# Optimization experiments

Hardware: AMD Instinct MI355X
Metric: run time of the kernel (lower is better)

The kernel has to match this reference:

```python
import jax, jax.numpy as jnp
import numpy as np

BLOCK = 32  # GGUF Q8_0 block size: one scale per 32 int8 quants


def setup_inputs() -> dict:
    key = jax.random.key(0)
    k1, k2, k3, k4 = jax.random.split(key, 4)
    B, S, D_IN, D_OUT = 2, 2048, 4096, 16384
    x = jax.random.normal(k1, (B, S, D_IN), dtype=jnp.float32)
    # Stored quantized weights: unsigned byte codes in [0,255]; dequant as (q-128)*scale
    weight_q = jax.random.randint(k2, (D_OUT, D_IN), 0, 255, dtype=jnp.int32)
    # One positive scale per 32-element block along in_features
    scales = jax.random.uniform(k3, (D_OUT, D_IN // BLOCK), dtype=jnp.float32) * 0.02 + 1e-3
    bias = jax.random.normal(k4, (D_OUT,), dtype=jnp.float32)
    return {"x": x, "weight_q": weight_q, "scales": scales, "bias": bias}


def _dequant(weight_q, scales):
    # weight_q: [O, I] int codes, scales: [O, I/BLOCK] -> fp weight [O, I]
    O, I = weight_q.shape
    q = (weight_q.astype(jnp.float32) - 128.0).reshape(O, I // BLOCK, BLOCK)
    return (q * scales[:, :, None]).reshape(O, I)


def reference(x, weight_q, scales, bias):
    # Fused dequant + matmul: y = x @ dequant(W).T + bias
    w = _dequant(weight_q, scales)  # [O, I]
    y = jnp.einsum("bsi,oi->bso", x, w)
    return y + bias
```

## Files before the change

### kernel.cpp

```cpp
#include <hip/hip_runtime.h>
#include <hip/hip_bf16.h>

typedef __attribute__((ext_vector_type(8))) short short8;
typedef __attribute__((ext_vector_type(4))) float f32x4;
typedef __attribute__((ext_vector_type(16))) float f32x16;

#define AS1 __attribute__((address_space(1)))
#define AS3 __attribute__((address_space(3)))

static __device__ __forceinline__ short f2bf(float f) {
    __hip_bfloat16 h = __float2bfloat16(f);
    union { __hip_bfloat16 h; short s; } u;
    u.h = h;
    return u.s;
}


__global__ __launch_bounds__(256) void prepack_w_kernel(const int* __restrict__ wq,
                                                        const float* __restrict__ scales,
                                                        short* __restrict__ Wb,
                                                        long total8) {
    long i = (long)blockIdx.x * 256 + threadIdx.x;
    if (i >= total8) return;
    const int4* p = (const int4*)wq + i * 2;
    int4 q0 = p[0], q1 = p[1];
    float s = scales[(i * 8) >> 5];
    short8 v;
    v[0] = f2bf((float)(q0.x - 128) * s);
    v[1] = f2bf((float)(q0.y - 128) * s);
    v[2] = f2bf((float)(q0.z - 128) * s);
    v[3] = f2bf((float)(q0.w - 128) * s);
    v[4] = f2bf((float)(q1.x - 128) * s);
    v[5] = f2bf((float)(q1.y - 128) * s);
    v[6] = f2bf((float)(q1.z - 128) * s);
    v[7] = f2bf((float)(q1.w - 128) * s);
    ((short8*)Wb)[i] = v;
}

__global__ __launch_bounds__(256) void prepack_x_kernel(const float* __restrict__ x,
                                                        short* __restrict__ Xb,
                                                        long total8) {
    long i = (long)blockIdx.x * 256 + threadIdx.x;
    if (i >= total8) return;
    const float4* p = (const float4*)x + i * 2;
    float4 f0 = p[0], f1 = p[1];
    short8 v;
    v[0] = f2bf(f0.x); v[1] = f2bf(f0.y); v[2] = f2bf(f0.z); v[3] = f2bf(f0.w);
    v[4] = f2bf(f1.x); v[5] = f2bf(f1.y); v[6] = f2bf(f1.z); v[7] = f2bf(f1.w);
    ((short8*)Xb)[i] = v;
}

__global__ __launch_bounds__(512, 2)
void gemm256_kernel(const float* __restrict__ bias,
                    const short* __restrict__ Xb, const short* __restrict__ Wb,
                    float* __restrict__ out, int M, int N, int K) {
    __shared__ alignas(16) short As[4 * 8192];
    __shared__ alignas(16) short Bs[4 * 8192];

    const int nM = M >> 8, nN = N >> 8;
    int bid = blockIdx.x;
    {
        int nwg = nM * nN;
        if ((nwg & 7) == 0) bid = (bid & 7) * (nwg >> 3) + (bid >> 3);
    }
    int pm, pn;
    {
        const int G = 8;
        if ((nN % G) == 0) {
            int per = nM * G;
            int grp = bid / per, in = bid % per;
            pn = grp * G + (in % G);
            pm = in / G;
        } else { pn = bid % nN; pm = bid / nN; }
    }

    const int tid  = threadIdx.x;
    const int lane = tid & 63;
    const int wid  = tid >> 6;
    const int wm   = wid >> 2;
    const int wn   = wid & 3;
    const int l31  = lane & 31;
    const int l5   = lane >> 5;
    const int lx   = lane & 7;

    const long bm = (long)pm << 8, bn = (long)pn << 8;
    const long Kl = K;
    const int  NT = K >> 6;

    const int aslot0 = wm * 8192,        aslot1 = (2 + wm) * 8192;
    const int bslot0 = (wn >> 1) * 8192 + ((wn & 1) * 64) * 64;
    const int bslot1 = bslot0 + 2 * 8192;
    const int frow   = l31 * 64;
    const int sgk0 = ((0 + l5) ^ lx) * 8;
    const int sgk1 = ((2 + l5) ^ lx) * 8;
    const int sgk2 = ((4 + l5) ^ lx) * 8;
    const int sgk3 = ((6 + l5) ^ lx) * 8;

    const int chnk    = wid * 1024;
    const int srowrel = wid * 16 + (lane >> 3);
    const int scol    = ((lane & 7) ^ (lane >> 3)) * 8;

    const short* aS00 = Xb + (bm + 0   + srowrel + 0) * Kl + scol;
    const short* aS01 = Xb + (bm + 0   + srowrel + 8) * Kl + scol;
    const short* aS10 = Xb + (bm + 128 + srowrel + 0) * Kl + scol;
    const short* aS11 = Xb + (bm + 128 + srowrel + 8) * Kl + scol;
    const short* bS00 = Wb + (bn + 0   + srowrel + 0) * Kl + scol;
    const short* bS01 = Wb + (bn + 0   + srowrel + 8) * Kl + scol;
    const short* bS10 = Wb + (bn + 128 + srowrel + 0) * Kl + scol;
    const short* bS11 = Wb + (bn + 128 + srowrel + 8) * Kl + scol;

#define STGA(H, PARL, OFF) {                                                          \
    __builtin_amdgcn_global_load_lds((const AS1 void*)(aS##H##0 + (OFF)),             \
        (AS3 void*)&As[((PARL) * 2 + (H)) * 8192 + chnk], 16, 0, 0);                  \
    __builtin_amdgcn_global_load_lds((const AS1 void*)(aS##H##1 + (OFF)),             \
        (AS3 void*)&As[((PARL) * 2 + (H)) * 8192 + chnk + 512], 16, 0, 0); }
#define STGB(H, PARL, OFF) {                                                          \
    __builtin_amdgcn_global_load_lds((const AS1 void*)(bS##H##0 + (OFF)),             \
        (AS3 void*)&Bs[((PARL) * 2 + (H)) * 8192 + chnk], 16, 0, 0);                  \
    __builtin_amdgcn_global_load_lds((const AS1 void*)(bS##H##1 + (OFF)),             \
        (AS3 void*)&Bs[((PARL) * 2 + (H)) * 8192 + chnk + 512], 16, 0, 0); }

#define RDA(BUF, ASLOT, SG) {                                                         \
    BUF[0] = *(const short8*)&As[(ASLOT) + 0 * 2048 + frow + (SG)];                   \
    BUF[1] = *(const short8*)&As[(ASLOT) + 1 * 2048 + frow + (SG)];                   \
    BUF[2] = *(const short8*)&As[(ASLOT) + 2 * 2048 + frow + (SG)];                   \
    BUF[3] = *(const short8*)&As[(ASLOT) + 3 * 2048 + frow + (SG)]; }

#define LDB_ALL(BSLOT) {                                                              \
    bfr[0][0] = *(const short8*)&Bs[(BSLOT) + 0 * 2048 + frow + sgk0];                \
    bfr[0][1] = *(const short8*)&Bs[(BSLOT) + 1 * 2048 + frow + sgk0];                \
    bfr[1][0] = *(const short8*)&Bs[(BSLOT) + 0 * 2048 + frow + sgk1];                \
    bfr[1][1] = *(const short8*)&Bs[(BSLOT) + 1 * 2048 + frow + sgk1];                \
    bfr[2][0] = *(const short8*)&Bs[(BSLOT) + 0 * 2048 + frow + sgk2];                \
    bfr[2][1] = *(const short8*)&Bs[(BSLOT) + 1 * 2048 + frow + sgk2];                \
    bfr[3][0] = *(const short8*)&Bs[(BSLOT) + 0 * 2048 + frow + sgk3];                \
    bfr[3][1] = *(const short8*)&Bs[(BSLOT) + 1 * 2048 + frow + sgk3]; }

#define MFMA8(S, ABUF) { __builtin_amdgcn_s_setprio(1);                               \
    _Pragma("unroll") for (int mb = 0; mb < 4; ++mb) {                                \
        acc[mb][0] = __builtin_amdgcn_mfma_f32_32x32x16_bf16(                         \
            ABUF[mb], bfr[S][0], acc[mb][0], 0, 0, 0);                                \
        acc[mb][1] = __builtin_amdgcn_mfma_f32_32x32x16_bf16(                         \
            ABUF[mb], bfr[S][1], acc[mb][1], 0, 0, 0); }                              \
    __builtin_amdgcn_s_setprio(0); }

#define BAR  { __builtin_amdgcn_s_barrier(); __builtin_amdgcn_sched_barrier(0); }
#define WLGN(n) { asm volatile("s_waitcnt lgkmcnt(" #n ")" ::: "memory");             \
                  __builtin_amdgcn_sched_barrier(0); }
#define VMC(n)  asm volatile("s_waitcnt vmcnt(" #n ")" ::: "memory")

#define TILE(ASLOT, BSLOT, NASLOT, APAR_N, BPAR_T, OFF_A, OFF_B, DO_A, DO_B, LAST, DRAIN0) { \
                                                                             \
    LDB_ALL(BSLOT);                                                                   \
    RDA(akB, ASLOT, sgk1);                                                            \
    if (DO_A) STGA(0, APAR_N, OFF_A);                                                 \
    WLGN(10);                                                                         \
    MFMA8(0, akA);                                                                    \
                                                                             \
    RDA(akA, ASLOT, sgk2);                                                            \
    if (DO_A) STGA(1, APAR_N, OFF_A);                                                 \
    WLGN(4);                                                                          \
    MFMA8(1, akB);                                                                    \
    BAR;                                                                              \
                                                                             \
    RDA(akB, ASLOT, sgk3);                                                            \
    if (DO_B) STGB(0, BPAR_T, OFF_B);                                                 \
    WLGN(4);                                                                          \
    MFMA8(2, akA);                                                                    \
                                                                             \
    if (DO_B) STGB(1, BPAR_T, OFF_B);                                                 \
    WLGN(0);                                                                          \
    MFMA8(3, akB);                                                                    \
    if (!(LAST)) {                                                                    \
        if (DRAIN0) { VMC(0); } else { VMC(2); }                                      \
        BAR;                                                                          \
        RDA(akA, NASLOT, sgk0);                                                       \
    } }

    f32x16 acc[4][2];
#pragma unroll
    for (int mb = 0; mb < 4; ++mb)
#pragma unroll
        for (int nb = 0; nb < 2; ++nb)
#pragma unroll
            for (int r = 0; r < 16; ++r) acc[mb][nb][r] = 0.f;

    short8 akA[4], akB[4], bfr[4][2];

    STGB(0, 0, 0); STGB(1, 0, 0);
    STGA(0, 0, 0); STGA(1, 0, 0);
    STGB(0, 1, 64); STGB(1, 1, 64);
    VMC(4);
    BAR;
    RDA(akA, aslot0, sgk0);

    for (int t = 0; t + 3 < NT; t += 2) {
        const long o1 = ((long)t + 1) << 6;
        const long o2 = o1 + 64;
        const long o3 = o2 + 64;
        TILE(aslot0, bslot0, aslot1, 1, 0, o1, o2, true, true, false, false);
        TILE(aslot1, bslot1, aslot0, 0, 1, o2, o3, true, true, false, false);
    }
    {
        const long o1 = ((long)NT - 1) << 6;
        TILE(aslot0, bslot0, aslot1, 1, 0, o1, 0, true, false, false, true);
        TILE(aslot1, bslot1, aslot0, 0, 1, 0, 0, false, false, true, false);
    }

#pragma unroll
    for (int nb = 0; nb < 2; ++nb) {
        long col = bn + wn * 64 + nb * 32 + l31;
        float bv = bias[col];
#pragma unroll
        for (int mb = 0; mb < 4; ++mb) {
            long rowb = bm + wm * 128 + mb * 32 + 4 * l5;
#pragma unroll
            for (int r = 0; r < 16; ++r) {
                long row = rowb + (r & 3) + 8 * (r >> 2);
                out[row * (long)N + col] = acc[mb][nb][r] + bv;
            }
        }
    }
#undef STGA
#undef STGB
#undef RDA
#undef LDB_ALL
#undef MFMA8
#undef BAR
#undef WLGN
#undef VMC
#undef TILE
}


template <bool PRE_A, bool PRE_B>
__global__ __launch_bounds__(256, 2)
void gemm_kernel(const float* __restrict__ x, const int* __restrict__ wq,
                 const float* __restrict__ scales, const float* __restrict__ bias,
                 const short* __restrict__ Xb, const short* __restrict__ Wb,
                 float* __restrict__ out, int M, int N, int K) {
    constexpr int BM = 128, BN = 128, BK = 64;
    __shared__ alignas(16) short As[BM * BK];
    __shared__ alignas(16) short Bs[BN * BK];

    const int nM = M / BM, nN = N / BN;
    int bid = blockIdx.x;
    int pm, pn;
    const int G = 8;
    if ((nN % G) == 0) {
        int per = nM * G;
        int grp = bid / per;
        int in  = bid % per;
        pn = grp * G + (in % G);
        pm = in / G;
    } else {
        pn = bid % nN;
        pm = bid / nN;
    }

    const int tid  = threadIdx.x;
    const int lane = tid & 63;
    const int wv   = tid >> 6;
    const int wm   = (wv >> 1) * 64;
    const int wn   = (wv & 1) * 64;
    const int q    = lane >> 4;
    const int l15  = lane & 15;
    const int sxor = lane & 7;

    const long bm = (long)pm * BM, bn = (long)pn * BN;

    f32x4 acc[4][4];
#pragma unroll
    for (int i = 0; i < 4; ++i)
#pragma unroll
        for (int j = 0; j < 4; ++j) acc[i][j] = (f32x4){0.f, 0.f, 0.f, 0.f};

    const int srow = tid >> 3;
    const int scg  = tid & 7;

    const int sg0   = q ^ sxor;
    const int aOff0 = (wm + l15) * 64 + sg0 * 8;
    const int aOff1 = (wm + l15) * 64 + (sg0 ^ 4) * 8;
    const int bOff0 = (wn + l15) * 64 + sg0 * 8;
    const int bOff1 = (wn + l15) * 64 + (sg0 ^ 4) * 8;

    const int prRow  = lane >> 3;
    const int prGsrc = (lane & 7) ^ (lane >> 3);

    for (int k0 = 0; k0 < K; k0 += BK) {
        if constexpr (PRE_A) {
#pragma unroll
            for (int i = 0; i < 4; ++i) {
                int r = wv * 32 + i * 8 + prRow;
                const short* src = Xb + (bm + r) * (long)K + k0 + prGsrc * 8;
                __builtin_amdgcn_global_load_lds((const AS1 void*)src,
                                                 (AS3 void*)&As[(wv * 32 + i * 8) * 64],
                                                 16, 0, 0);
            }
        } else {
#pragma unroll
            for (int i = 0; i < 4; ++i) {
                int r = i * 32 + srow;
                const float4* p = (const float4*)(x + (bm + r) * (long)K + k0 + scg * 8);
                float4 f0 = p[0], f1 = p[1];
                short8 v;
                v[0] = f2bf(f0.x); v[1] = f2bf(f0.y); v[2] = f2bf(f0.z); v[3] = f2bf(f0.w);
                v[4] = f2bf(f1.x); v[5] = f2bf(f1.y); v[6] = f2bf(f1.z); v[7] = f2bf(f1.w);
                int sg = scg ^ (r & 7);
                *(short8*)&As[r * 64 + sg * 8] = v;
            }
        }
        if constexpr (PRE_B) {
#pragma unroll
            for (int i = 0; i < 4; ++i) {
                int r = wv * 32 + i * 8 + prRow;
                const short* src = Wb + (bn + r) * (long)K + k0 + prGsrc * 8;
                __builtin_amdgcn_global_load_lds((const AS1 void*)src,
                                                 (AS3 void*)&Bs[(wv * 32 + i * 8) * 64],
                                                 16, 0, 0);
            }
        } else {
#pragma unroll
            for (int i = 0; i < 4; ++i) {
                int r = i * 32 + srow;
                const int4* p = (const int4*)(wq + (bn + r) * (long)K + k0 + scg * 8);
                int4 q0 = p[0], q1 = p[1];
                float s = scales[(bn + r) * (long)(K >> 5) + ((k0 + scg * 8) >> 5)];
                short8 v;
                v[0] = f2bf((float)(q0.x - 128) * s);
                v[1] = f2bf((float)(q0.y - 128) * s);
                v[2] = f2bf((float)(q0.z - 128) * s);
                v[3] = f2bf((float)(q0.w - 128) * s);
                v[4] = f2bf((float)(q1.x - 128) * s);
                v[5] = f2bf((float)(q1.y - 128) * s);
                v[6] = f2bf((float)(q1.z - 128) * s);
                v[7] = f2bf((float)(q1.w - 128) * s);
                int sg = scg ^ (r & 7);
                *(short8*)&Bs[r * 64 + sg * 8] = v;
            }
        }
        __syncthreads();

#pragma unroll
        for (int kk = 0; kk < 2; ++kk) {
            short8 a[4], b[4];
            const int aBase = kk ? aOff1 : aOff0;
            const int bBase = kk ? bOff1 : bOff0;
#pragma unroll
            for (int mi = 0; mi < 4; ++mi) a[mi] = *(const short8*)&As[aBase + mi * 16 * 64];
#pragma unroll
            for (int nj = 0; nj < 4; ++nj) b[nj] = *(const short8*)&Bs[bBase + nj * 16 * 64];
#pragma unroll
            for (int mi = 0; mi < 4; ++mi)
#pragma unroll
                for (int nj = 0; nj < 4; ++nj)
                    acc[mi][nj] = __builtin_amdgcn_mfma_f32_16x16x32_bf16(
                        a[mi], b[nj], acc[mi][nj], 0, 0, 0);
        }
        __syncthreads();
    }

#pragma unroll
    for (int nj = 0; nj < 4; ++nj) {
        long col = bn + wn + nj * 16 + l15;
        float bv = bias[col];
#pragma unroll
        for (int mi = 0; mi < 4; ++mi) {
            long row = bm + wm + mi * 16 + q * 4;
#pragma unroll
            for (int r2 = 0; r2 < 4; ++r2)
                out[(row + r2) * (long)N + col] = acc[mi][nj][r2] + bv;
        }
    }
}


extern "C" void kernel_launch(void* const* d_in, const int* in_sizes, int n_in,
                              void* d_out, int out_size, void* d_ws, size_t ws_size,
                              hipStream_t stream) {
    const float* x      = (const float*)d_in[0];
    const int*   wq     = (const int*)d_in[1];
    const float* scales = (const float*)d_in[2];
    const float* bias   = (const float*)d_in[3];
    float*       out    = (float*)d_out;

    const long N = (long)in_sizes[3];
    const long K = (long)in_sizes[1] / N;
    const long M = (long)in_sizes[0] / K;

    const size_t needW = (size_t)N * K * sizeof(short);
    const size_t needX = (size_t)M * K * sizeof(short);

    short* Wb = (short*)d_ws;
    short* Xb = Wb + (size_t)N * K;

    const bool preB = (d_ws != nullptr) && ws_size >= needW;
    const bool preA = preB && ws_size >= (needW + needX);

    if (preB) {
        long t8 = N * K / 8;
        prepack_w_kernel<<<dim3((unsigned)((t8 + 255) / 256)), dim3(256), 0, stream>>>(
            wq, scales, Wb, t8);
    }
    if (preA) {
        long t8 = M * K / 8;
        prepack_x_kernel<<<dim3((unsigned)((t8 + 255) / 256)), dim3(256), 0, stream>>>(
            x, Xb, t8);
    }

    const long NTl = K / 64;
    const bool big = preA && (M % 256 == 0) && (N % 256 == 0) && (K % 64 == 0) &&
                     (NTl >= 4) && (NTl % 2 == 0);

    if (big) {
        dim3 grid((unsigned)((M / 256) * (N / 256))), block(512);
        gemm256_kernel<<<grid, block, 0, stream>>>(bias, Xb, Wb, out, (int)M, (int)N, (int)K);
    } else {
        dim3 grid((unsigned)((M / 128) * (N / 128))), block(256);
        if (preA)
            gemm_kernel<true, true><<<grid, block, 0, stream>>>(x, wq, scales, bias, Xb, Wb,
                                                                out, (int)M, (int)N, (int)K);
        else if (preB)
            gemm_kernel<false, true><<<grid, block, 0, stream>>>(x, wq, scales, bias, Xb, Wb,
                                                                 out, (int)M, (int)N, (int)K);
        else
            gemm_kernel<false, false><<<grid, block, 0, stream>>>(x, wq, scales, bias, Xb, Wb,
                                                                  out, (int)M, (int)N, (int)K);
    }
}
```

Before: 628.1 us.

## Replace double-buffered A fragments with single buffer and barrier-synchronized MFMA phases

Restructures the main-loop tile schedule of the 256x256 kernel. A-fragment register double buffering (akA/akB with a prefetch of the next tile) is replaced by one ak buffer loaded right before each MFMA group. Each group is now bracketed by workgroup barriers and full LDS waits, which lowers VGPR pressure and lines waves up in a ping-pong style. The cost is that LDS reads are no longer overlapped with MFMAs, and there are many more barriers per tile.

```diff
diff --git a/kernel.cpp b/kernel.cpp
--- a/kernel.cpp
+++ b/kernel.cpp
@@ -120,11 +120,11 @@
     __builtin_amdgcn_global_load_lds((const AS1 void*)(bS##H##1 + (OFF)),             \
         (AS3 void*)&Bs[((PARL) * 2 + (H)) * 8192 + chnk + 512], 16, 0, 0); }
 
-#define RDA(BUF, ASLOT, SG) {                                                         \
-    BUF[0] = *(const short8*)&As[(ASLOT) + 0 * 2048 + frow + (SG)];                   \
-    BUF[1] = *(const short8*)&As[(ASLOT) + 1 * 2048 + frow + (SG)];                   \
-    BUF[2] = *(const short8*)&As[(ASLOT) + 2 * 2048 + frow + (SG)];                   \
-    BUF[3] = *(const short8*)&As[(ASLOT) + 3 * 2048 + frow + (SG)]; }
+#define RDA(ASLOT, SG) {                                                              \
+    ak[0] = *(const short8*)&As[(ASLOT) + 0 * 2048 + frow + (SG)];                    \
+    ak[1] = *(const short8*)&As[(ASLOT) + 1 * 2048 + frow + (SG)];                    \
+    ak[2] = *(const short8*)&As[(ASLOT) + 2 * 2048 + frow + (SG)];                    \
+    ak[3] = *(const short8*)&As[(ASLOT) + 3 * 2048 + frow + (SG)]; }
 
 #define LDB_ALL(BSLOT) {                                                              \
     bfr[0][0] = *(const short8*)&Bs[(BSLOT) + 0 * 2048 + frow + sgk0];                \
@@ -136,45 +136,39 @@
     bfr[3][0] = *(const short8*)&Bs[(BSLOT) + 0 * 2048 + frow + sgk3];                \
     bfr[3][1] = *(const short8*)&Bs[(BSLOT) + 1 * 2048 + frow + sgk3]; }
 
-#define MFMA8(S, ABUF) { __builtin_amdgcn_s_setprio(1);                               \
+#define MFMA8(S) { __builtin_amdgcn_s_setprio(1);                                     \
     _Pragma("unroll") for (int mb = 0; mb < 4; ++mb) {                                \
         acc[mb][0] = __builtin_amdgcn_mfma_f32_32x32x16_bf16(                         \
-            ABUF[mb], bfr[S][0], acc[mb][0], 0, 0, 0);                                \
+            ak[mb], bfr[S][0], acc[mb][0], 0, 0, 0);                                  \
         acc[mb][1] = __builtin_amdgcn_mfma_f32_32x32x16_bf16(                         \
-            ABUF[mb], bfr[S][1], acc[mb][1], 0, 0, 0); }                              \
+            ak[mb], bfr[S][1], acc[mb][1], 0, 0, 0); }                                \
     __builtin_amdgcn_s_setprio(0); }
 
-#define BAR  { __builtin_amdgcn_s_barrier(); __builtin_amdgcn_sched_barrier(0); }
+#define BAR  __builtin_amdgcn_s_barrier()
 #define WLGN(n) { asm volatile("s_waitcnt lgkmcnt(" #n ")" ::: "memory");             \
                   __builtin_amdgcn_sched_barrier(0); }
 #define VMC(n)  asm volatile("s_waitcnt vmcnt(" #n ")" ::: "memory")
 
-#define TILE(ASLOT, BSLOT, NASLOT, APAR_N, BPAR_T, OFF_A, OFF_B, DO_A, DO_B, LAST, DRAIN0) { \
+#define TILE32(ASLOT, BSLOT, APAR_N, BPAR_T, OFF_A, OFF_B, DO_A, DO_B, LAST, DRAIN0) { \
                                                                              \
-    LDB_ALL(BSLOT);                                                                   \
-    RDA(akB, ASLOT, sgk1);                                                            \
+    RDA(ASLOT, sgk0); LDB_ALL(BSLOT);                                                 \
     if (DO_A) STGA(0, APAR_N, OFF_A);                                                 \
-    WLGN(10);                                                                         \
-    MFMA8(0, akA);                                                                    \
+    WLGN(8); BAR; WLGN(0); MFMA8(0); BAR;                                             \
                                                                              \
-    RDA(akA, ASLOT, sgk2);                                                            \
+    RDA(ASLOT, sgk1);                                                                 \
     if (DO_A) STGA(1, APAR_N, OFF_A);                                                 \
-    WLGN(4);                                                                          \
-    MFMA8(1, akB);                                                                    \
-    BAR;                                                                              \
+    BAR; WLGN(0); MFMA8(1); BAR;                                                      \
                                                                              \
-    RDA(akB, ASLOT, sgk3);                                                            \
+    RDA(ASLOT, sgk2);                                                                 \
     if (DO_B) STGB(0, BPAR_T, OFF_B);                                                 \
-    WLGN(4);                                                                          \
-    MFMA8(2, akA);                                                                    \
+    BAR; WLGN(0); MFMA8(2); BAR;                                                      \
                                                                              \
+    RDA(ASLOT, sgk3);                                                                 \
     if (DO_B) STGB(1, BPAR_T, OFF_B);                                                 \
-    WLGN(0);                                                                          \
-    MFMA8(3, akB);                                                                    \
+    BAR; WLGN(0); MFMA8(3);                                                           \
     if (!(LAST)) {                                                                    \
-        if (DRAIN0) { VMC(0); } else { VMC(2); }                                      \
+        if (DRAIN0) { VMC(0); } else { VMC(4); }                                      \
         BAR;                                                                          \
-        RDA(akA, NASLOT, sgk0);                                                       \
     } }
 
     f32x16 acc[4][2];
@@ -185,26 +179,25 @@
 #pragma unroll
             for (int r = 0; r < 16; ++r) acc[mb][nb][r] = 0.f;
 
-    short8 akA[4], akB[4], bfr[4][2];
+    short8 ak[4], bfr[4][2];
 
     STGB(0, 0, 0); STGB(1, 0, 0);
     STGA(0, 0, 0); STGA(1, 0, 0);
     STGB(0, 1, 64); STGB(1, 1, 64);
     VMC(4);
     BAR;
-    RDA(akA, aslot0, sgk0);
 
     for (int t = 0; t + 3 < NT; t += 2) {
         const long o1 = ((long)t + 1) << 6;
         const long o2 = o1 + 64;
         const long o3 = o2 + 64;
-        TILE(aslot0, bslot0, aslot1, 1, 0, o1, o2, true, true, false, false);
-        TILE(aslot1, bslot1, aslot0, 0, 1, o2, o3, true, true, false, false);
+        TILE32(aslot0, bslot0, 1, 0, o1, o2, true, true, false, false);
+        TILE32(aslot1, bslot1, 0, 1, o2, o3, true, true, false, false);
     }
     {
         const long o1 = ((long)NT - 1) << 6;
-        TILE(aslot0, bslot0, aslot1, 1, 0, o1, 0, true, false, false, true);
-        TILE(aslot1, bslot1, aslot0, 0, 1, 0, 0, false, false, true, false);
+        TILE32(aslot0, bslot0, 1, 0, o1, 0, true, false, false, true);
+        TILE32(aslot1, bslot1, 0, 1, 0, 0, false, false, true, false);
     }
 
 #pragma unroll
@@ -229,7 +222,7 @@
 #undef BAR
 #undef WLGN
 #undef VMC
-#undef TILE
+#undef TILE32
 }
 
 
```

Result: no change. 625.4 us (-0.4%).
